# Kernel tuning notes

Measured on AMD Instinct MI355X. Metric: run time of the kernel, lower is better.

Reference implementation:

```python
import jax, jax.numpy as jnp
import numpy as np

N = 50000
C_IN = 64
C_OUT = 64
K = 16
EPS = 1e-5


def _bn(x, g, b, m, v):
    # eval-mode BatchNorm1d over last dim
    return (x - m) * jax.lax.rsqrt(v + EPS) * g + b


def setup_inputs() -> dict:
    key = jax.random.key(0)
    ks = jax.random.split(key, 24)
    def lin(i, fan_in, fan_out):
        s = 1.0 / np.sqrt(fan_in)
        W = jax.random.uniform(ks[i], (fan_in, fan_out), jnp.float32, -s, s)
        b = jax.random.uniform(ks[i + 1], (fan_out,), jnp.float32, -s, s)
        return W, b
    Wq, bq = lin(0, C_IN, C_OUT)
    Wk, bk = lin(2, C_IN, C_OUT)
    Wv, bv = lin(4, C_IN, C_OUT)
    Wp, b_p = lin(6, 3, C_OUT)
    Wg1, bg1 = lin(8, C_OUT, C_OUT)
    Wg2, bg2 = lin(10, C_OUT, C_OUT)
    Wo, bo = lin(12, C_OUT, C_OUT)
    def bn_params(i):
        g = jax.random.uniform(ks[i], (C_OUT,), jnp.float32, 0.5, 1.5)
        b = jax.random.normal(ks[i + 1], (C_OUT,), jnp.float32) * 0.1
        m = jax.random.normal(ks[i + 2], (C_OUT,), jnp.float32) * 0.1
        v = jax.random.uniform(ks[i + 3], (C_OUT,), jnp.float32, 0.5, 1.5)
        return g, b, m, v
    bnp_g, bnp_b, bnp_m, bnp_v = bn_params(14)
    bng_g, bng_b, bng_m, bng_v = bn_params(18)
    points = jax.random.normal(ks[22], (N, 3), jnp.float32)
    features = jax.random.normal(ks[23], (N, C_IN), jnp.float32)
    grouped_indices = jax.random.randint(jax.random.fold_in(key, 7), (N, K), 0, N, jnp.int64 if jax.config.jax_enable_x64 else jnp.int32)
    return dict(points=points, features=features, grouped_indices=grouped_indices,
                Wq=Wq, bq=bq, Wk=Wk, bk=bk, Wv=Wv, bv=bv, Wp=Wp, b_p=b_p,
                bnp_g=bnp_g, bnp_b=bnp_b, bnp_m=bnp_m, bnp_v=bnp_v,
                Wg1=Wg1, bg1=bg1, bng_g=bng_g, bng_b=bng_b, bng_m=bng_m, bng_v=bng_v,
                Wg2=Wg2, bg2=bg2, Wo=Wo, bo=bo)


def reference(points, features, grouped_indices,
              Wq, bq, Wk, bk, Wv, bv, Wp, b_p,
              bnp_g, bnp_b, bnp_m, bnp_v,
              Wg1, bg1, bng_g, bng_b, bng_m, bng_v,
              Wg2, bg2, Wo, bo):
    q = features @ Wq + bq                      # (N, C)
    k = features @ Wk + bk
    v = features @ Wv + bv
    gpts = points[grouped_indices]              # (N, K, 3) gather
    gk = k[grouped_indices]                     # (N, K, C)
    gv = v[grouped_indices]                     # (N, K, C)
    rel = gpts - points[:, None, :]             # (N, K, 3)
    p = jax.nn.relu(_bn(rel @ Wp + b_p, bnp_g, bnp_b, bnp_m, bnp_v))  # (N, K, C)
    a = q[:, None, :] - gk + p                  # (N, K, C)
    h = jax.nn.relu(_bn(a @ Wg1 + bg1, bng_g, bng_b, bng_m, bng_v)) @ Wg2 + bg2
    attn = jax.nn.softmax(h, axis=1)            # softmax over neighbor axis
    out = jnp.sum((gv + p) * attn, axis=1) @ Wo + bo  # (N, C)
    return out
```

## Files before the change

kernel.cpp:

```cpp
#include <hip/hip_runtime.h>
#include <hip/hip_bf16.h>

#define EPSV 1e-5f
#define TW 4

typedef __attribute__((ext_vector_type(8))) short s8v;
typedef __attribute__((ext_vector_type(4))) float f4v;

struct InP {
  const float *points, *features; const int* gidx;
  const float *Wq,*bq,*Wk,*bk,*Wv,*bv,*Wp,*b_p;
  const float *bnp_g,*bnp_b,*bnp_m,*bnp_v;
  const float *Wg1,*bg1,*bng_g,*bng_b,*bng_m,*bng_v;
  const float *Wg2,*bg2,*Wo,*bo;
  float* out; int N;
};
struct WS {
  unsigned short *qW1;
  unsigned short *kvT;
  unsigned short *WAf, *Wkf, *Wvf, *W1f, *W2f, *Wof;
  unsigned short *Wpf;
  float *bq1F, *bpF;
};

__device__ __forceinline__ unsigned short f2bf(float x){
  __hip_bfloat16 h = __float2bfloat16(x);
  unsigned short u; __builtin_memcpy(&u, &h, 2); return u;
}
__device__ __forceinline__ float bf2f(unsigned short s){
  union{unsigned u; float f;} c; c.u = ((unsigned)s) << 16; return c.f;
}
__device__ __forceinline__ unsigned pk2(float x, float y){
  __hip_bfloat162 h = __float22bfloat162_rn(make_float2(x, y));
  unsigned u; __builtin_memcpy(&u, &h, 4); return u;
}
__device__ __forceinline__ s8v pack8(f4v x0, f4v x1){
  s8v r;
  ((unsigned*)&r)[0] = pk2(x0[0], x0[1]);
  ((unsigned*)&r)[1] = pk2(x0[2], x0[3]);
  ((unsigned*)&r)[2] = pk2(x1[0], x1[1]);
  ((unsigned*)&r)[3] = pk2(x1[2], x1[3]);
  return r;
}
__device__ __forceinline__ s8v pack8sub(f4v x0, f4v x1, s8v k){
  s8v r;
  ((unsigned*)&r)[0] = pk2(x0[0]-bf2f((unsigned short)k[0]), x0[1]-bf2f((unsigned short)k[1]));
  ((unsigned*)&r)[1] = pk2(x0[2]-bf2f((unsigned short)k[2]), x0[3]-bf2f((unsigned short)k[3]));
  ((unsigned*)&r)[2] = pk2(x1[0]-bf2f((unsigned short)k[4]), x1[1]-bf2f((unsigned short)k[5]));
  ((unsigned*)&r)[3] = pk2(x1[2]-bf2f((unsigned short)k[6]), x1[3]-bf2f((unsigned short)k[7]));
  return r;
}

__global__ void __launch_bounds__(256) prep_kernel(InP P, WS W){
  const int g = blockIdx.x*256 + threadIdx.x;
  const int e = g >> 3, j = g & 7;
  const int f = e >> 6, L = e & 63;
  const int ks = f & 1, nt = f >> 1;
  const int n = nt*16 + (L & 15);
  const int k = ks*32 + ((L >> 4) << 3) + j;
  const float sg = P.bng_g[n] * rsqrtf(P.bng_v[n] + EPSV);
  W.W1f[e*8+j] = f2bf(P.Wg1[k*64+n] * sg);
  W.W2f[e*8+j] = f2bf(P.Wg2[k*64+n]);
  W.Wof[e*8+j] = f2bf(P.Wo [k*64+n]);
  W.Wkf[e*8+j] = f2bf(P.Wk [k*64+n]);
  W.Wvf[e*8+j] = f2bf(P.Wv [k*64+n]);
  float acc = 0.f;
  #pragma unroll 8
  for (int d = 0; d < 64; d++) acc += P.Wq[k*64+d] * P.Wg1[d*64+n];
  W.WAf[e*8+j] = f2bf(acc * sg);
  if (g < 2048){
    int ep = g >> 3;
    int ntp = ep >> 6, Lp = ep & 63;
    int np_ = ntp*16 + (Lp & 15);
    int kp = ((Lp >> 4) << 3) + j;
    float sp = P.bnp_g[np_] * rsqrtf(P.bnp_v[np_] + EPSV);
    W.Wpf[ep*8+j] = f2bf(kp < 3 ? P.Wp[kp*64+np_]*sp : 0.f);
  }
  if (g < 64){
    float sgt = P.bng_g[g] * rsqrtf(P.bng_v[g] + EPSV);
    float spt = P.bnp_g[g] * rsqrtf(P.bnp_v[g] + EPSV);
    float acc2 = 0.f;
    for (int d = 0; d < 64; d++) acc2 += P.bq[d] * P.Wg1[d*64+g];
    W.bq1F[g] = acc2*sgt + P.bg1[g]*sgt + P.bng_b[g] - P.bng_m[g]*sgt;
    W.bpF[g]  = P.b_p[g]*spt + P.bnp_b[g] - P.bnp_m[g]*spt;
  }
}

__global__ void __launch_bounds__(256) qkv_kernel(InP P, WS W){
  const int tid = threadIdx.x;
  const int wid = tid >> 6, l = tid & 63;
  const int cl = l & 15, q = l >> 4;
  const int TILES = (P.N + 15) >> 4;
  const int task = blockIdx.x * TW + wid;
  if (task >= TILES) return;
  const int i0 = task * 16;
  int row = i0 + cl; if (row > P.N - 1) row = P.N - 1;
  const float* fr = P.features + (size_t)row*64 + q*8;
  f4v x0 = *(const f4v*)fr;
  f4v x1 = *(const f4v*)(fr + 4);
  s8v fa0 = pack8(x0, x1);
  x0 = *(const f4v*)(fr + 32);
  x1 = *(const f4v*)(fr + 36);
  s8v fa1 = pack8(x0, x1);

  auto doMat = [&](const unsigned short* Bf_, const float* biasPtr,
                   unsigned short* outPtr, int stride){
    const s8v* Bf = (const s8v*)Bf_;
    #pragma unroll
    for (int nt = 0; nt < 4; nt++){
      float bn = biasPtr[nt*16 + cl];
      f4v ci = { bn, bn, bn, bn };
      f4v c = __builtin_amdgcn_mfma_f32_16x16x32_bf16(fa0, Bf[(2*nt+0)*64 + l], ci, 0, 0, 0);
      c = __builtin_amdgcn_mfma_f32_16x16x32_bf16(fa1, Bf[(2*nt+1)*64 + l], c, 0, 0, 0);
      #pragma unroll
      for (int r = 0; r < 4; r++){
        int rg = i0 + q*4 + r;
        if (rg < P.N) outPtr[(size_t)rg*stride + nt*16 + cl] = f2bf(c[r]);
      }
    }
  };
  doMat(W.WAf, W.bq1F, W.qW1,      64);
  doMat(W.Wkf, P.bk,   W.kvT,     128);
  doMat(W.Wvf, P.bv,   W.kvT + 64,128);
}

__global__ void __launch_bounds__(256, 2) main_kernel(InP P, WS W){
  __shared__ __align__(16) float Sp[TW][16*68];
  __shared__ __align__(16) unsigned short Vg[TW][16*72];
  __shared__ __align__(16) unsigned short PreB[TW][16*72];
  __shared__ __align__(16) int sI[TW][256];
  const int tid = threadIdx.x;
  const int wid = tid >> 6, l = tid & 63;
  const int cl = l & 15, q = l >> 4;
  const int TILES = (P.N + 15) >> 4;
  const int task = blockIdx.x * TW + wid;
  if (task >= TILES) return;
  const int i0 = task * 16;
  float* Spw = Sp[wid];
  unsigned short* Vgw = Vg[wid];
  unsigned short* PreBw = PreB[wid];
  int* sIw = sI[wid];

  {
    long base = (long)i0*16 + l*4;
    long maxb = (long)P.N*16 - 4;
    if (base > maxb) base = maxb;
    int4 gi = *(const int4*)(P.gidx + base);
    *(int4*)&sIw[l*4] = gi;
  }

  s8v w1f[8], w2f[8], wpf[4];
  {
    const s8v* W1p = (const s8v*)W.W1f;
    const s8v* W2p = (const s8v*)W.W2f;
    const s8v* Wpp = (const s8v*)W.Wpf;
    #pragma unroll
    for (int f = 0; f < 8; f++){ w1f[f] = W1p[f*64 + l]; w2f[f] = W2p[f*64 + l]; }
    #pragma unroll
    for (int f = 0; f < 4; f++) wpf[f] = Wpp[f*64 + l];
  }
  float bp4[4], b24[4];
  #pragma unroll
  for (int nt = 0; nt < 4; nt++){ bp4[nt] = W.bpF[nt*16 + cl]; b24[nt] = P.bg2[nt*16 + cl]; }

  int nidx = sIw[cl];
  s8v ngk0, ngk1, ngv0, ngv1;
  {
    const s8v* kv = (const s8v*)(W.kvT + (size_t)nidx*128);
    ngk0 = kv[q]; ngk1 = kv[4+q]; ngv0 = kv[8+q]; ngv1 = kv[12+q];
  }
  float ngx=0.f, ngy=0.f, ngz=0.f;
  if (l < 16){ const float* gp = P.points + (size_t)nidx*3; ngx=gp[0]; ngy=gp[1]; ngz=gp[2]; }
  float ncx = P.points[(size_t)i0*3+0];
  float ncy = P.points[(size_t)i0*3+1];
  float ncz = P.points[(size_t)i0*3+2];
  float nq0, nq1, nq2, nq3;
  {
    const unsigned short* qr = W.qW1 + (size_t)i0*64;
    nq0 = bf2f(qr[cl]); nq1 = bf2f(qr[16+cl]); nq2 = bf2f(qr[32+cl]); nq3 = bf2f(qr[48+cl]);
  }

  #pragma unroll 1
  for (int pt = 0; pt < 16; pt++){
    s8v gk0=ngk0, gk1=ngk1, gv0=ngv0, gv1=ngv1;
    float gx=ngx, gy=ngy, gz=ngz, cx=ncx, cy=ncy, cz=ncz;
    float qc0=nq0, qc1=nq1, qc2=nq2, qc3=nq3;

    *(s8v*)&Vgw[cl*72 + q*8]      = gv0;
    *(s8v*)&Vgw[cl*72 + 32 + q*8] = gv1;

    s8v ap;
    ((unsigned*)&ap)[0] = pk2(gx-cx, gy-cy);
    ((unsigned*)&ap)[1] = pk2(gz-cz, 0.f);
    ((unsigned*)&ap)[2] = 0u; ((unsigned*)&ap)[3] = 0u;
    f4v pc[4];
    #pragma unroll
    for (int nt = 0; nt < 4; nt++){
      f4v ci = { bp4[nt], bp4[nt], bp4[nt], bp4[nt] };
      pc[nt] = __builtin_amdgcn_mfma_f32_16x16x32_bf16(ap, wpf[nt], ci, 0, 0, 0);
    }
    unsigned pcp[8];
    #pragma unroll
    for (int nt = 0; nt < 4; nt++){
      #pragma unroll
      for (int r = 0; r < 4; r++){
        pc[nt][r] = fmaxf(pc[nt][r], 0.f);
        Spw[(q*4+r)*68 + nt*16 + cl] = pc[nt][r];
      }
      pcp[nt*2+0] = pk2(pc[nt][0], pc[nt][1]);
      pcp[nt*2+1] = pk2(pc[nt][2], pc[nt][3]);
    }

    {
      int np = (pt + 1) & 15;
      nidx = sIw[np*16 + cl];
      const s8v* kv = (const s8v*)(W.kvT + (size_t)nidx*128);
      ngk0 = kv[q]; ngk1 = kv[4+q]; ngv0 = kv[8+q]; ngv1 = kv[12+q];
      if (l < 16){ const float* gp = P.points + (size_t)nidx*3; ngx=gp[0]; ngy=gp[1]; ngz=gp[2]; }
      int ii = i0 + np; if (ii > P.N - 1) ii = P.N - 1;
      ncx = P.points[(size_t)ii*3+0];
      ncy = P.points[(size_t)ii*3+1];
      ncz = P.points[(size_t)ii*3+2];
      const unsigned short* qr = W.qW1 + (size_t)ii*64;
      nq0 = bf2f(qr[cl]); nq1 = bf2f(qr[16+cl]); nq2 = bf2f(qr[32+cl]); nq3 = bf2f(qr[48+cl]);
    }

    s8v af0, af1;
    {
      const f4v* pr = (const f4v*)&Spw[cl*68 + q*8];
      af0 = pack8sub(pr[0], pr[1], gk0);
      pr = (const f4v*)&Spw[cl*68 + 32 + q*8];
      af1 = pack8sub(pr[0], pr[1], gk1);
    }

    f4v tc[4];
    #pragma unroll
    for (int nt = 0; nt < 4; nt++){
      float qcn = (nt==0) ? qc0 : (nt==1) ? qc1 : (nt==2) ? qc2 : qc3;
      f4v ci = { qcn, qcn, qcn, qcn };
      tc[nt] = __builtin_amdgcn_mfma_f32_16x16x32_bf16(af0, w1f[2*nt+0], ci, 0, 0, 0);
      tc[nt] = __builtin_amdgcn_mfma_f32_16x16x32_bf16(af1, w1f[2*nt+1], tc[nt], 0, 0, 0);
      #pragma unroll
      for (int r = 0; r < 4; r++) tc[nt][r] = fmaxf(tc[nt][r], 0.f);
    }

    #pragma unroll
    for (int nt = 0; nt < 4; nt++)
      #pragma unroll
      for (int r = 0; r < 4; r++)
        Spw[(q*4+r)*68 + nt*16 + cl] = tc[nt][r];
    s8v tf0, tf1;
    {
      const f4v* pr = (const f4v*)&Spw[cl*68 + q*8];
      tf0 = pack8(pr[0], pr[1]);
      pr = (const f4v*)&Spw[cl*68 + 32 + q*8];
      tf1 = pack8(pr[0], pr[1]);
    }

    f4v hc[4];
    #pragma unroll
    for (int nt = 0; nt < 4; nt++){
      f4v ci = { b24[nt], b24[nt], b24[nt], b24[nt] };
      hc[nt] = __builtin_amdgcn_mfma_f32_16x16x32_bf16(tf0, w2f[2*nt+0], ci, 0, 0, 0);
      hc[nt] = __builtin_amdgcn_mfma_f32_16x16x32_bf16(tf1, w2f[2*nt+1], hc[nt], 0, 0, 0);
    }

    float pre4[4];
    #pragma unroll
    for (int nt = 0; nt < 4; nt++){
      float mx = fmaxf(fmaxf(hc[nt][0], hc[nt][1]), fmaxf(hc[nt][2], hc[nt][3]));
      mx = fmaxf(mx, __shfl_xor(mx, 16, 64));
      mx = fmaxf(mx, __shfl_xor(mx, 32, 64));
      float s = 0.f;
      #pragma unroll
      for (int r = 0; r < 4; r++){ float e2 = __expf(hc[nt][r] - mx); hc[nt][r] = e2; s += e2; }
      s += __shfl_xor(s, 16, 64);
      s += __shfl_xor(s, 32, 64);
      float inv = __builtin_amdgcn_rcpf(s);
      float p01lo = bf2f((unsigned short)(pcp[nt*2+0] & 0xffff));
      float p01hi = bf2f((unsigned short)(pcp[nt*2+0] >> 16));
      float p23lo = bf2f((unsigned short)(pcp[nt*2+1] & 0xffff));
      float p23hi = bf2f((unsigned short)(pcp[nt*2+1] >> 16));
      float pv[4] = { p01lo, p01hi, p23lo, p23hi };
      float acc = 0.f;
      #pragma unroll
      for (int r = 0; r < 4; r++){
        float vv = bf2f(Vgw[(q*4+r)*72 + nt*16 + cl]);
        acc = fmaf(hc[nt][r], vv + pv[r], acc);
      }
      acc += __shfl_xor(acc, 16, 64);
      acc += __shfl_xor(acc, 32, 64);
      pre4[nt] = acc * inv;
    }
    float sa = (l & 16) ? pre4[1] : pre4[0];
    float sb = (l & 16) ? pre4[3] : pre4[2];
    PreBw[pt*72 + l] = f2bf((l & 32) ? sb : sa);
  }

  s8v wof[8];
  {
    const s8v* Wop = (const s8v*)W.Wof;
    #pragma unroll
    for (int f = 0; f < 8; f++) wof[f] = Wop[f*64 + l];
  }
  s8v ef0 = *(const s8v*)&PreBw[cl*72 + q*8];
  s8v ef1 = *(const s8v*)&PreBw[cl*72 + 32 + q*8];
  #pragma unroll
  for (int nt = 0; nt < 4; nt++){
    float bn = P.bo[nt*16 + cl];
    f4v ci = { bn, bn, bn, bn };
    f4v oc = __builtin_amdgcn_mfma_f32_16x16x32_bf16(ef0, wof[2*nt+0], ci, 0, 0, 0);
    oc = __builtin_amdgcn_mfma_f32_16x16x32_bf16(ef1, wof[2*nt+1], oc, 0, 0, 0);
    #pragma unroll
    for (int r = 0; r < 4; r++){
      int rg = i0 + q*4 + r;
      if (rg < P.N) P.out[(size_t)rg*64 + nt*16 + cl] = oc[r];
    }
  }
}

extern "C" void kernel_launch(void* const* d_in, const int* in_sizes, int n_in,
                              void* d_out, int out_size, void* d_ws, size_t ws_size,
                              hipStream_t stream){
  InP P;
  P.points   = (const float*)d_in[0];
  P.features = (const float*)d_in[1];
  P.gidx     = (const int*)d_in[2];
  P.Wq  = (const float*)d_in[3];  P.bq  = (const float*)d_in[4];
  P.Wk  = (const float*)d_in[5];  P.bk  = (const float*)d_in[6];
  P.Wv  = (const float*)d_in[7];  P.bv  = (const float*)d_in[8];
  P.Wp  = (const float*)d_in[9];  P.b_p = (const float*)d_in[10];
  P.bnp_g = (const float*)d_in[11]; P.bnp_b = (const float*)d_in[12];
  P.bnp_m = (const float*)d_in[13]; P.bnp_v = (const float*)d_in[14];
  P.Wg1 = (const float*)d_in[15]; P.bg1 = (const float*)d_in[16];
  P.bng_g = (const float*)d_in[17]; P.bng_b = (const float*)d_in[18];
  P.bng_m = (const float*)d_in[19]; P.bng_v = (const float*)d_in[20];
  P.Wg2 = (const float*)d_in[21]; P.bg2 = (const float*)d_in[22];
  P.Wo  = (const float*)d_in[23]; P.bo  = (const float*)d_in[24];
  P.out = (float*)d_out;
  const int N = in_sizes[0] / 3;
  P.N = N;

  WS W;
  char* w = (char*)d_ws;
  W.qW1 = (unsigned short*)w; w += (size_t)N*64*2;
  W.kvT = (unsigned short*)w; w += (size_t)N*128*2;
  W.WAf = (unsigned short*)w; w += 8*64*8*2;
  W.Wkf = (unsigned short*)w; w += 8*64*8*2;
  W.Wvf = (unsigned short*)w; w += 8*64*8*2;
  W.W1f = (unsigned short*)w; w += 8*64*8*2;
  W.W2f = (unsigned short*)w; w += 8*64*8*2;
  W.Wof = (unsigned short*)w; w += 8*64*8*2;
  W.Wpf = (unsigned short*)w; w += 4*64*8*2;
  W.bq1F = (float*)w; w += 256;
  W.bpF  = (float*)w; w += 256;

  const int TILES = (N + 15) / 16;
  const int grid = (TILES + TW - 1) / TW;
  hipLaunchKernelGGL(prep_kernel, dim3(16),   dim3(256), 0, stream, P, W);
  hipLaunchKernelGGL(qkv_kernel,  dim3(grid), dim3(256), 0, stream, P, W);
  hipLaunchKernelGGL(main_kernel, dim3(grid), dim3(256), 0, stream, P, W);
}
```

Baseline: 218.2 us.

## Store LDS transpose scratch as bf16, double-buffer per point, unroll loop by two

```diff
diff --git a/kernel.cpp b/kernel.cpp
--- a/kernel.cpp
+++ b/kernel.cpp
@@ -3,6 +3,7 @@
 
 #define EPSV 1e-5f
 #define TW 4
+#define SPD 76
 
 typedef __attribute__((ext_vector_type(8))) short s8v;
 typedef __attribute__((ext_vector_type(4))) float f4v;
@@ -42,12 +43,14 @@
   ((unsigned*)&r)[3] = pk2(x1[2], x1[3]);
   return r;
 }
-__device__ __forceinline__ s8v pack8sub(f4v x0, f4v x1, s8v k){
+__device__ __forceinline__ s8v sub8bf(s8v p, s8v k){
   s8v r;
-  ((unsigned*)&r)[0] = pk2(x0[0]-bf2f((unsigned short)k[0]), x0[1]-bf2f((unsigned short)k[1]));
-  ((unsigned*)&r)[1] = pk2(x0[2]-bf2f((unsigned short)k[2]), x0[3]-bf2f((unsigned short)k[3]));
-  ((unsigned*)&r)[2] = pk2(x1[0]-bf2f((unsigned short)k[4]), x1[1]-bf2f((unsigned short)k[5]));
-  ((unsigned*)&r)[3] = pk2(x1[2]-bf2f((unsigned short)k[6]), x1[3]-bf2f((unsigned short)k[7]));
+  #pragma unroll
+  for (int t = 0; t < 4; t++){
+    float a0 = bf2f((unsigned short)p[2*t+0]) - bf2f((unsigned short)k[2*t+0]);
+    float a1 = bf2f((unsigned short)p[2*t+1]) - bf2f((unsigned short)k[2*t+1]);
+    ((unsigned*)&r)[t] = pk2(a0, a1);
+  }
   return r;
 }
 
@@ -125,9 +128,9 @@
 }
 
 __global__ void __launch_bounds__(256, 2) main_kernel(InP P, WS W){
-  __shared__ __align__(16) float Sp[TW][16*68];
-  __shared__ __align__(16) unsigned short Vg[TW][16*72];
-  __shared__ __align__(16) unsigned short PreB[TW][16*72];
+  __shared__ __align__(16) unsigned short Sp[TW][2][16*SPD];
+  __shared__ __align__(16) unsigned short Vg[TW][2][16*SPD];
+  __shared__ __align__(16) unsigned short PreB[TW][16*SPD];
   __shared__ __align__(16) int sI[TW][256];
   const int tid = threadIdx.x;
   const int wid = tid >> 6, l = tid & 63;
@@ -136,8 +139,6 @@
   const int task = blockIdx.x * TW + wid;
   if (task >= TILES) return;
   const int i0 = task * 16;
-  float* Spw = Sp[wid];
-  unsigned short* Vgw = Vg[wid];
   unsigned short* PreBw = PreB[wid];
   int* sIw = sI[wid];
 
@@ -180,14 +181,16 @@
     nq0 = bf2f(qr[cl]); nq1 = bf2f(qr[16+cl]); nq2 = bf2f(qr[32+cl]); nq3 = bf2f(qr[48+cl]);
   }
 
-  #pragma unroll 1
+  #pragma unroll 2
   for (int pt = 0; pt < 16; pt++){
+    unsigned short* Spw = Sp[wid][pt & 1];
+    unsigned short* Vgw = Vg[wid][pt & 1];
     s8v gk0=ngk0, gk1=ngk1, gv0=ngv0, gv1=ngv1;
     float gx=ngx, gy=ngy, gz=ngz, cx=ncx, cy=ncy, cz=ncz;
     float qc0=nq0, qc1=nq1, qc2=nq2, qc3=nq3;
 
-    *(s8v*)&Vgw[cl*72 + q*8]      = gv0;
-    *(s8v*)&Vgw[cl*72 + 32 + q*8] = gv1;
+    *(s8v*)&Vgw[cl*SPD + q*8]      = gv0;
+    *(s8v*)&Vgw[cl*SPD + 32 + q*8] = gv1;
 
     s8v ap;
     ((unsigned*)&ap)[0] = pk2(gx-cx, gy-cy);
@@ -205,7 +208,7 @@
       #pragma unroll
       for (int r = 0; r < 4; r++){
         pc[nt][r] = fmaxf(pc[nt][r], 0.f);
-        Spw[(q*4+r)*68 + nt*16 + cl] = pc[nt][r];
+        Spw[(q*4+r)*SPD + nt*16 + cl] = f2bf(pc[nt][r]);
       }
       pcp[nt*2+0] = pk2(pc[nt][0], pc[nt][1]);
       pcp[nt*2+1] = pk2(pc[nt][2], pc[nt][3]);
@@ -227,10 +230,10 @@
 
     s8v af0, af1;
     {
-      const f4v* pr = (const f4v*)&Spw[cl*68 + q*8];
-      af0 = pack8sub(pr[0], pr[1], gk0);
-      pr = (const f4v*)&Spw[cl*68 + 32 + q*8];
-      af1 = pack8sub(pr[0], pr[1], gk1);
+      s8v p0 = *(const s8v*)&Spw[cl*SPD + q*8];
+      s8v p1 = *(const s8v*)&Spw[cl*SPD + 32 + q*8];
+      af0 = sub8bf(p0, gk0);
+      af1 = sub8bf(p1, gk1);
     }
 
     f4v tc[4];
@@ -248,14 +251,9 @@
     for (int nt = 0; nt < 4; nt++)
       #pragma unroll
       for (int r = 0; r < 4; r++)
-        Spw[(q*4+r)*68 + nt*16 + cl] = tc[nt][r];
-    s8v tf0, tf1;
-    {
-      const f4v* pr = (const f4v*)&Spw[cl*68 + q*8];
-      tf0 = pack8(pr[0], pr[1]);
-      pr = (const f4v*)&Spw[cl*68 + 32 + q*8];
-      tf1 = pack8(pr[0], pr[1]);
-    }
+        Spw[(q*4+r)*SPD + nt*16 + cl] = f2bf(tc[nt][r]);
+    s8v tf0 = *(const s8v*)&Spw[cl*SPD + q*8];
+    s8v tf1 = *(const s8v*)&Spw[cl*SPD + 32 + q*8];
 
     f4v hc[4];
     #pragma unroll
@@ -274,9 +272,6 @@
       float s = 0.f;
       #pragma unroll
       for (int r = 0; r < 4; r++){ float e2 = __expf(hc[nt][r] - mx); hc[nt][r] = e2; s += e2; }
-      s += __shfl_xor(s, 16, 64);
-      s += __shfl_xor(s, 32, 64);
-      float inv = __builtin_amdgcn_rcpf(s);
       float p01lo = bf2f((unsigned short)(pcp[nt*2+0] & 0xffff));
       float p01hi = bf2f((unsigned short)(pcp[nt*2+0] >> 16));
       float p23lo = bf2f((unsigned short)(pcp[nt*2+1] & 0xffff));
@@ -285,16 +280,18 @@
       float acc = 0.f;
       #pragma unroll
       for (int r = 0; r < 4; r++){
-        float vv = bf2f(Vgw[(q*4+r)*72 + nt*16 + cl]);
+        float vv = bf2f(Vgw[(q*4+r)*SPD + nt*16 + cl]);
         acc = fmaf(hc[nt][r], vv + pv[r], acc);
       }
+      s += __shfl_xor(s, 16, 64);
+      s += __shfl_xor(s, 32, 64);
       acc += __shfl_xor(acc, 16, 64);
       acc += __shfl_xor(acc, 32, 64);
-      pre4[nt] = acc * inv;
+      pre4[nt] = acc * __builtin_amdgcn_rcpf(s);
     }
     float sa = (l & 16) ? pre4[1] : pre4[0];
     float sb = (l & 16) ? pre4[3] : pre4[2];
-    PreBw[pt*72 + l] = f2bf((l & 32) ? sb : sa);
+    PreBw[pt*SPD + l] = f2bf((l & 32) ? sb : sa);
   }
 
   s8v wof[8];
@@ -303,8 +300,8 @@
     #pragma unroll
     for (int f = 0; f < 8; f++) wof[f] = Wop[f*64 + l];
   }
-  s8v ef0 = *(const s8v*)&PreBw[cl*72 + q*8];
-  s8v ef1 = *(const s8v*)&PreBw[cl*72 + 32 + q*8];
+  s8v ef0 = *(const s8v*)&PreBw[cl*SPD + q*8];
+  s8v ef1 = *(const s8v*)&PreBw[cl*SPD + 32 + q*8];
   #pragma unroll
   for (int nt = 0; nt < 4; nt++){
     float bn = P.bo[nt*16 + cl];
```

Measured after the change: 231.8 us. +6.2%, slower.
